# Optimization experiments

Hardware: AMD Instinct MI355X
Metric: run time of the kernel (lower is better)

Reference implementation:

```python
import jax, jax.numpy as jnp
import numpy as np

HEAD_SIZE = 64
N_EMBD = 1024
BLOCK_SIZE = 2048


def setup_inputs() -> dict:
    key = jax.random.key(0)
    ks = jax.random.split(key, 7)
    B, T = 4, 2048
    s = 1.0 / np.sqrt(N_EMBD)
    return {
        "x": jax.random.normal(ks[0], (B, T, N_EMBD), dtype=jnp.float32),
        "Wq": jax.random.normal(ks[1], (N_EMBD, HEAD_SIZE), dtype=jnp.float32) * s,
        "bq": jnp.zeros((HEAD_SIZE,), dtype=jnp.float32),
        "Wk": jax.random.normal(ks[2], (N_EMBD, HEAD_SIZE), dtype=jnp.float32) * s,
        "bk": jnp.zeros((HEAD_SIZE,), dtype=jnp.float32),
        "Wv": jax.random.normal(ks[3], (N_EMBD, HEAD_SIZE), dtype=jnp.float32) * s,
        "bv": jnp.zeros((HEAD_SIZE,), dtype=jnp.float32),
    }


def reference(x, Wq, bq, Wk, bk, Wv, bv):
    # x: [B, T, n_embd]
    B, T, _ = x.shape
    q = x @ Wq + bq  # [B, T, H]
    k = x @ Wk + bk
    v = x @ Wv + bv
    # Faithful to source: divides by head_size**(-0.5) == multiplies by sqrt(head_size)
    scale = jnp.float32(HEAD_SIZE) ** 0.5
    scores = jnp.einsum("bqh,bkh->bqk", q, k) * scale  # [B, T, T]
    causal = jnp.tril(jnp.ones((T, T), dtype=bool))
    scores = jnp.where(causal, scores, -jnp.inf)
    attn = jax.nn.softmax(scores, axis=-1)  # dropout p=0.0 (eval)
    out = jnp.einsum("bqk,bkh->bqh", attn, v)  # [B, T, H]
    return out
```

## Files before the change

kernel.cpp:

```cpp
#include <hip/hip_runtime.h>
#include <math.h>

#define NE 1024
#define HS 64
#define TT 2048
#define QSC 11.541560327111707f

typedef __bf16    v8bf __attribute__((ext_vector_type(8)));
typedef _Float16  v8h  __attribute__((ext_vector_type(8)));
typedef float     v4f  __attribute__((ext_vector_type(4)));

#define MFMA_BF(a, b, c)  __builtin_amdgcn_mfma_f32_16x16x32_bf16((a), (b), (c), 0, 0, 0)
#define MFMA_F16(a, b, c) __builtin_amdgcn_mfma_f32_16x16x32_f16((a), (b), (c), 0, 0, 0)

__device__ __forceinline__ void gl_lds16(const void* g, void* l) {
    __builtin_amdgcn_global_load_lds(
        (const __attribute__((address_space(1))) unsigned int*)g,
        (__attribute__((address_space(3))) unsigned int*)l, 16, 0, 0);
}

__global__ __launch_bounds__(256) void prep_w(
    const float* __restrict__ Wq, const float* __restrict__ Wk,
    const float* __restrict__ Wv, char* __restrict__ imgW)
{
    __shared__ float t[64][65];
    const int bx = blockIdx.x, by = blockIdx.y;
    const float* W = (by == 0) ? Wq : ((by == 1) ? Wk : Wv);
    const int tid = threadIdx.x;
    const int cc = tid & 63, r4 = tid >> 6;
    #pragma unroll
    for (int p = 0; p < 16; ++p) {
        const int k = p * 4 + r4;
        t[k][cc] = W[(size_t)(bx * 64 + k) * HS + cc];
    }
    __syncthreads();
    #pragma unroll
    for (int e = 0; e < 4; ++e) {
        const int chunk = tid + e * 256;
        const int s2   = chunk >> 9;
        const int rem  = chunk & 511;
        const int ctl  = rem >> 7;
        const int rem2 = rem & 127;
        const int pl   = rem2 >> 6;
        const int rem3 = rem2 & 63;
        const int c    = rem3 >> 2;
        const int p16  = rem3 & 3;
        const int kb   = s2 * 32 + ((p16 ^ (c & 3)) << 3);
        const int ncol = ctl * 16 + c;
        v8bf o;
        #pragma unroll
        for (int j = 0; j < 8; ++j) {
            const float v = t[kb + j][ncol];
            const __bf16 h = (__bf16)v;
            o[j] = pl ? (__bf16)(v - (float)h) : h;
        }
        *(v8bf*)(imgW + (size_t)(bx * 2 + s2) * 24576
                 + (by * 4 + ctl) * 2048 + pl * 1024 + c * 64 + p16 * 16) = o;
    }
}

__global__ __launch_bounds__(512, 2) void proj(
    const float* __restrict__ x, const char* __restrict__ imgW,
    const float* __restrict__ bq, const float* __restrict__ bk,
    const float* __restrict__ bv,
    __bf16* __restrict__ qh, __bf16* __restrict__ ql,
    __bf16* __restrict__ kh, __bf16* __restrict__ kl,
    _Float16* __restrict__ vt)
{
    __shared__ __align__(16) char sbuf[2][28672];

    const int tid = threadIdx.x, lane = tid & 63, w = tid >> 6;
    const int rg = w & 1, cg = w >> 1;
    const int quad = lane >> 4, l16 = lane & 15;
    const int m0 = blockIdx.x * 32;

    const int xrow = tid >> 3;
    const int xc32 = ((tid & 7) >> 1) ^ (xrow & 3);
    const float* gx = x + (size_t)(m0 + xrow) * NE + xc32 * 8 + (tid & 1) * 4;
    const char*  gw = imgW + (size_t)tid * 16;

    v4f acc[3];
    #pragma unroll
    for (int i = 0; i < 3; ++i) acc[i] = (v4f){0.f, 0.f, 0.f, 0.f};

    #define STAGE(ks, b)  do {                                        \
        char* xb_ = sbuf[(b)];                                        \
        if (tid < 256) gl_lds16(gx + (ks) * 32, xb_ + tid * 16);      \
        const char* gws_ = gw + (size_t)(ks) * 24576;                 \
        gl_lds16(gws_,         xb_ + 4096  + tid * 16);               \
        gl_lds16(gws_ + 8192,  xb_ + 12288 + tid * 16);               \
        gl_lds16(gws_ + 16384, xb_ + 20480 + tid * 16);               \
    } while (0)

    STAGE(0, 0);
    __syncthreads();

    for (int ks = 0; ks < 32; ++ks) {
        const int b = ks & 1;
        if (ks < 31) STAGE(ks + 1, b ^ 1);

        const char* xb = sbuf[b];
        const char* wb = xb + 4096;
        const int rl = rg * 16 + l16;
        const int pA = quad ^ (rl & 3);
        const float4 a0 = *(const float4*)(xb + rl * 128 + pA * 32);
        const float4 a1 = *(const float4*)(xb + rl * 128 + pA * 32 + 16);
        const float av[8] = {a0.x, a0.y, a0.z, a0.w, a1.x, a1.y, a1.z, a1.w};
        v8bf ah, al;
        #pragma unroll
        for (int i = 0; i < 8; ++i) {
            const __bf16 h = (__bf16)av[i];
            ah[i] = h;
            al[i] = (__bf16)(av[i] - (float)h);
        }
        const int wo = l16 * 64 + ((quad ^ (l16 & 3)) << 4);
        #pragma unroll
        for (int j = 0; j < 3; ++j) {
            const char* base = wb + (cg * 3 + j) * 2048 + wo;
            const v8bf bh = *(const v8bf*)(base);
            const v8bf bl = *(const v8bf*)(base + 1024);
            acc[j] = MFMA_BF(ah, bh, acc[j]);
            acc[j] = MFMA_BF(ah, bl, acc[j]);
            acc[j] = MFMA_BF(al, bh, acc[j]);
        }
        __syncthreads();
    }
    #undef STAGE

    #pragma unroll
    for (int j = 0; j < 3; ++j) {
        const int n = cg * 48 + j * 16 + l16;
        const float bias = (n < 64) ? bq[n] : ((n < 128) ? bk[n - 64] : bv[n - 128]);
        #pragma unroll
        for (int reg = 0; reg < 4; ++reg) {
            const int row = m0 + rg * 16 + quad * 4 + reg;
            const float v = acc[j][reg] + bias;
            if (n < 64) {
                const float s = v * QSC;
                const __bf16 hh = (__bf16)s;
                qh[(size_t)row * HS + n] = hh;
                ql[(size_t)row * HS + n] = (__bf16)(s - (float)hh);
            } else if (n < 128) {
                const __bf16 hh = (__bf16)v;
                kh[(size_t)row * HS + n - 64] = hh;
                kl[(size_t)row * HS + n - 64] = (__bf16)(v - (float)hh);
            } else {
                const int b = row >> 11, tt = row & 2047, hc = n - 128;
                vt[((size_t)(b * HS + hc)) * TT + tt] = (_Float16)v;
            }
        }
    }
}

__global__ __launch_bounds__(256) void attn(
    const __bf16* __restrict__ qh, const __bf16* __restrict__ ql,
    const __bf16* __restrict__ kh, const __bf16* __restrict__ kl,
    const _Float16* __restrict__ vt, float* __restrict__ out)
{
    __shared__ __align__(16) char smem_raw[4 * 16 * 68 * 4];
    _Float16* ps = (_Float16*)smem_raw;
    float*    os = (float*)smem_raw;
    __shared__ float sm[4][16], sl[4][16];

    const int tid = threadIdx.x, lane = tid & 63, w = tid >> 6;
    const int quad = lane >> 4, l16 = lane & 15;
    const int b = blockIdx.x & 3, qi = blockIdx.x >> 2;
    const int q0 = (127 - qi) * 16;

    const size_t qrow = ((size_t)b * TT + q0 + l16) * HS;
    const v8bf Qh0 = *(const v8bf*)(qh + qrow + quad * 8);
    const v8bf Qh1 = *(const v8bf*)(qh + qrow + 32 + quad * 8);
    const v8bf Ql0 = *(const v8bf*)(ql + qrow + quad * 8);
    const v8bf Ql1 = *(const v8bf*)(ql + qrow + 32 + quad * 8);

    const v8h vones = {(_Float16)1.f, (_Float16)1.f, (_Float16)1.f, (_Float16)1.f,
                       (_Float16)1.f, (_Float16)1.f, (_Float16)1.f, (_Float16)1.f};

    float mrow[4] = {-3e38f, -3e38f, -3e38f, -3e38f};
    v4f o[4], o4;
    #pragma unroll
    for (int i = 0; i < 4; ++i) o[i] = (v4f){0.f, 0.f, 0.f, 0.f};
    o4 = (v4f){0.f, 0.f, 0.f, 0.f};

    const int irow = q0 + quad * 4;
    const int ntk = (q0 + 16 + 63) >> 6;
    _Float16* pw = ps + w * (16 * 72);

    for (int t = w; t < ntk; t += 4) {
        const int j0 = t * 64;
        v8bf Kh[8], Kl[8];
        v8h  Vf[8];
        #pragma unroll
        for (int nt = 0; nt < 4; ++nt) {
            const size_t krow = ((size_t)b * TT + j0 + nt * 16 + l16) * HS;
            Kh[nt * 2]     = *(const v8bf*)(kh + krow + quad * 8);
            Kh[nt * 2 + 1] = *(const v8bf*)(kh + krow + 32 + quad * 8);
            Kl[nt * 2]     = *(const v8bf*)(kl + krow + quad * 8);
            Kl[nt * 2 + 1] = *(const v8bf*)(kl + krow + 32 + quad * 8);
        }
        #pragma unroll
        for (int nt = 0; nt < 4; ++nt) {
            const size_t vrow = ((size_t)(b * HS + nt * 16 + l16)) * TT + j0;
            Vf[nt * 2]     = *(const v8h*)(vt + vrow + quad * 8);
            Vf[nt * 2 + 1] = *(const v8h*)(vt + vrow + 32 + quad * 8);
        }

        v4f s[4];
        #pragma unroll
        for (int i = 0; i < 4; ++i) s[i] = (v4f){0.f, 0.f, 0.f, 0.f};
        #pragma unroll
        for (int nt = 0; nt < 4; ++nt) {
            s[nt] = MFMA_BF(Qh0, Kh[nt * 2],     s[nt]);
            s[nt] = MFMA_BF(Qh1, Kh[nt * 2 + 1], s[nt]);
            s[nt] = MFMA_BF(Qh0, Kl[nt * 2],     s[nt]);
            s[nt] = MFMA_BF(Qh1, Kl[nt * 2 + 1], s[nt]);
            s[nt] = MFMA_BF(Ql0, Kh[nt * 2],     s[nt]);
            s[nt] = MFMA_BF(Ql1, Kh[nt * 2 + 1], s[nt]);
        }

        float mx[4] = {-3e38f, -3e38f, -3e38f, -3e38f};
        #pragma unroll
        for (int nt = 0; nt < 4; ++nt)
            #pragma unroll
            for (int reg = 0; reg < 4; ++reg) {
                if (j0 + nt * 16 + l16 > irow + reg) s[nt][reg] = -3e38f;
                mx[reg] = fmaxf(mx[reg], s[nt][reg]);
            }
        #pragma unroll
        for (int off = 8; off; off >>= 1)
            #pragma unroll
            for (int reg = 0; reg < 4; ++reg)
                mx[reg] = fmaxf(mx[reg], __shfl_xor(mx[reg], off));

        float al[4];
        #pragma unroll
        for (int reg = 0; reg < 4; ++reg) {
            const float mn = fmaxf(mrow[reg], mx[reg]);
            al[reg] = exp2f(mrow[reg] - mn);
            mrow[reg] = mn;
        }
        #pragma unroll
        for (int nt = 0; nt < 4; ++nt)
            #pragma unroll
            for (int reg = 0; reg < 4; ++reg) {
                const float p = (j0 + nt * 16 + l16 > irow + reg)
                                    ? 0.f : exp2f(s[nt][reg] - mrow[reg]);
                pw[(quad * 4 + reg) * 72 + nt * 16 + l16] = (_Float16)p;
            }
        #pragma unroll
        for (int nt = 0; nt < 4; ++nt)
            #pragma unroll
            for (int reg = 0; reg < 4; ++reg)
                o[nt][reg] *= al[reg];
        #pragma unroll
        for (int reg = 0; reg < 4; ++reg)
            o4[reg] *= al[reg];

        v8h Pa0 = *(const v8h*)(pw + l16 * 72 + quad * 8);
        v8h Pa1 = *(const v8h*)(pw + l16 * 72 + 32 + quad * 8);
        #pragma unroll
        for (int nt = 0; nt < 4; ++nt) {
            o[nt] = MFMA_F16(Pa0, Vf[nt * 2],     o[nt]);
            o[nt] = MFMA_F16(Pa1, Vf[nt * 2 + 1], o[nt]);
        }
        o4 = MFMA_F16(Pa0, vones, o4);
        o4 = MFMA_F16(Pa1, vones, o4);
    }

    if (l16 == 0) {
        #pragma unroll
        for (int reg = 0; reg < 4; ++reg) {
            sm[w][quad * 4 + reg] = mrow[reg];
            sl[w][quad * 4 + reg] = o4[reg];
        }
    }
    __syncthreads();
    float sc[4];
    #pragma unroll
    for (int reg = 0; reg < 4; ++reg) {
        const int r = quad * 4 + reg;
        float M = sm[0][r];
        #pragma unroll
        for (int i = 1; i < 4; ++i) M = fmaxf(M, sm[i][r]);
        sc[reg] = exp2f(mrow[reg] - M);
    }
    float* ow = os + w * (16 * 68);
    #pragma unroll
    for (int nt = 0; nt < 4; ++nt)
        #pragma unroll
        for (int reg = 0; reg < 4; ++reg)
            ow[(quad * 4 + reg) * 68 + nt * 16 + l16] = o[nt][reg] * sc[reg];
    __syncthreads();

    #pragma unroll
    for (int kk = 0; kk < 4; ++kk) {
        const int m = w * 4 + kk;
        float M = sm[0][m];
        #pragma unroll
        for (int i = 1; i < 4; ++i) M = fmaxf(M, sm[i][m]);
        float L = 0.f, val = 0.f;
        #pragma unroll
        for (int i = 0; i < 4; ++i) {
            L   += sl[i][m] * exp2f(sm[i][m] - M);
            val += os[i * (16 * 68) + m * 68 + lane];
        }
        out[((size_t)b * TT + q0 + m) * HS + lane] = val / L;
    }
}

extern "C" void kernel_launch(void* const* d_in, const int* in_sizes, int n_in,
                              void* d_out, int out_size, void* d_ws, size_t ws_size,
                              hipStream_t stream)
{
    const float* x  = (const float*)d_in[0];
    const float* Wq = (const float*)d_in[1];
    const float* bq = (const float*)d_in[2];
    const float* Wk = (const float*)d_in[3];
    const float* bk = (const float*)d_in[4];
    const float* Wv = (const float*)d_in[5];
    const float* bv = (const float*)d_in[6];
    float* out = (float*)d_out;

    const int rows = in_sizes[0] / NE;
    char* p = (char*)d_ws;
    char* imgW = p;                           p += (size_t)32 * 24576;
    __bf16* qhb = (__bf16*)p;                 p += (size_t)rows * HS * 2;
    __bf16* qlb = (__bf16*)p;                 p += (size_t)rows * HS * 2;
    __bf16* khb = (__bf16*)p;                 p += (size_t)rows * HS * 2;
    __bf16* klb = (__bf16*)p;                 p += (size_t)rows * HS * 2;
    _Float16* vtb = (_Float16*)p;             p += (size_t)rows * HS * 2;

    prep_w<<<dim3(16, 3), 256, 0, stream>>>(Wq, Wk, Wv, imgW);
    proj<<<rows / 32, 512, 0, stream>>>(x, imgW, bq, bk, bv,
                                        qhb, qlb, khb, klb, vtb);
    attn<<<rows / 16, 256, 0, stream>>>(qhb, qlb, khb, klb, vtb, out);
}
```

Measured before the change: 147.8 us.

## Prefetch next K tile in attention and halve projection block size

The attention loop now double-buffers K tiles in registers, loading the next tile's K while the current tile's QK MFMAs and softmax run, so global load latency is hidden. It also adds a min-2-blocks launch bound to attn. The projection kernel is reshaped from 512-thread, 32-row blocks to 256-thread, 16-row blocks, doubling the grid and shrinking LDS per block. The extra K buffers raise register pressure, which could cut occupancy or cause spills, and smaller proj blocks reuse each staged weight tile across fewer rows.

After: 154.0 us. 4.2% more time.

```diff
diff --git a/kernel.cpp b/kernel.cpp
--- a/kernel.cpp
+++ b/kernel.cpp
@@ -59,7 +59,7 @@
     }
 }
 
-__global__ __launch_bounds__(512, 2) void proj(
+__global__ __launch_bounds__(256, 2) void proj(
     const float* __restrict__ x, const char* __restrict__ imgW,
     const float* __restrict__ bq, const float* __restrict__ bk,
     const float* __restrict__ bv,
@@ -67,12 +67,11 @@
     __bf16* __restrict__ kh, __bf16* __restrict__ kl,
     _Float16* __restrict__ vt)
 {
-    __shared__ __align__(16) char sbuf[2][28672];
-
-    const int tid = threadIdx.x, lane = tid & 63, w = tid >> 6;
-    const int rg = w & 1, cg = w >> 1;
+    __shared__ __align__(16) char sbuf[2][26624];
+
+    const int tid = threadIdx.x, lane = tid & 63, cg = tid >> 6;
     const int quad = lane >> 4, l16 = lane & 15;
-    const int m0 = blockIdx.x * 32;
+    const int m0 = blockIdx.x * 16;
 
     const int xrow = tid >> 3;
     const int xc32 = ((tid & 7) >> 1) ^ (xrow & 3);
@@ -83,13 +82,13 @@
     #pragma unroll
     for (int i = 0; i < 3; ++i) acc[i] = (v4f){0.f, 0.f, 0.f, 0.f};
 
-    #define STAGE(ks, b)  do {                                        \
-        char* xb_ = sbuf[(b)];                                        \
-        if (tid < 256) gl_lds16(gx + (ks) * 32, xb_ + tid * 16);      \
-        const char* gws_ = gw + (size_t)(ks) * 24576;                 \
-        gl_lds16(gws_,         xb_ + 4096  + tid * 16);               \
-        gl_lds16(gws_ + 8192,  xb_ + 12288 + tid * 16);               \
-        gl_lds16(gws_ + 16384, xb_ + 20480 + tid * 16);               \
+    #define STAGE(ks, b)  do {                                           \
+        char* xb_ = sbuf[(b)];                                           \
+        if (tid < 128) gl_lds16(gx + (ks) * 32, xb_ + tid * 16);         \
+        const char* gws_ = gw + (size_t)(ks) * 24576;                    \
+        _Pragma("unroll")                                                \
+        for (int j_ = 0; j_ < 6; ++j_)                                   \
+            gl_lds16(gws_ + j_ * 4096, xb_ + 2048 + tid * 16 + j_ * 4096); \
     } while (0)
 
     STAGE(0, 0);
@@ -100,8 +99,8 @@
         if (ks < 31) STAGE(ks + 1, b ^ 1);
 
         const char* xb = sbuf[b];
-        const char* wb = xb + 4096;
-        const int rl = rg * 16 + l16;
+        const char* wb = xb + 2048;
+        const int rl = l16;
         const int pA = quad ^ (rl & 3);
         const float4 a0 = *(const float4*)(xb + rl * 128 + pA * 32);
         const float4 a1 = *(const float4*)(xb + rl * 128 + pA * 32 + 16);
@@ -133,7 +132,7 @@
         const float bias = (n < 64) ? bq[n] : ((n < 128) ? bk[n - 64] : bv[n - 128]);
         #pragma unroll
         for (int reg = 0; reg < 4; ++reg) {
-            const int row = m0 + rg * 16 + quad * 4 + reg;
+            const int row = m0 + quad * 4 + reg;
             const float v = acc[j][reg] + bias;
             if (n < 64) {
                 const float s = v * QSC;
@@ -145,14 +144,14 @@
                 kh[(size_t)row * HS + n - 64] = hh;
                 kl[(size_t)row * HS + n - 64] = (__bf16)(v - (float)hh);
             } else {
-                const int b = row >> 11, tt = row & 2047, hc = n - 128;
-                vt[((size_t)(b * HS + hc)) * TT + tt] = (_Float16)v;
+                const int b2 = row >> 11, tt = row & 2047, hc = n - 128;
+                vt[((size_t)(b2 * HS + hc)) * TT + tt] = (_Float16)v;
             }
         }
     }
 }
 
-__global__ __launch_bounds__(256) void attn(
+__global__ __launch_bounds__(256, 2) void attn(
     const __bf16* __restrict__ qh, const __bf16* __restrict__ ql,
     const __bf16* __restrict__ kh, const __bf16* __restrict__ kl,
     const _Float16* __restrict__ vt, float* __restrict__ out)
@@ -186,38 +185,38 @@
     const int ntk = (q0 + 16 + 63) >> 6;
     _Float16* pw = ps + w * (16 * 72);
 
-    for (int t = w; t < ntk; t += 4) {
-        const int j0 = t * 64;
-        v8bf Kh[8], Kl[8];
-        v8h  Vf[8];
+    auto loadK = [&](v8bf (&Kh_)[8], v8bf (&Kl_)[8], int j0) {
         #pragma unroll
         for (int nt = 0; nt < 4; ++nt) {
             const size_t krow = ((size_t)b * TT + j0 + nt * 16 + l16) * HS;
-            Kh[nt * 2]     = *(const v8bf*)(kh + krow + quad * 8);
-            Kh[nt * 2 + 1] = *(const v8bf*)(kh + krow + 32 + quad * 8);
-            Kl[nt * 2]     = *(const v8bf*)(kl + krow + quad * 8);
-            Kl[nt * 2 + 1] = *(const v8bf*)(kl + krow + 32 + quad * 8);
-        }
+            Kh_[nt * 2]     = *(const v8bf*)(kh + krow + quad * 8);
+            Kh_[nt * 2 + 1] = *(const v8bf*)(kh + krow + 32 + quad * 8);
+            Kl_[nt * 2]     = *(const v8bf*)(kl + krow + quad * 8);
+            Kl_[nt * 2 + 1] = *(const v8bf*)(kl + krow + 32 + quad * 8);
+        }
+    };
+    auto loadV = [&](v8h (&Vf_)[8], int j0) {
         #pragma unroll
         for (int nt = 0; nt < 4; ++nt) {
             const size_t vrow = ((size_t)(b * HS + nt * 16 + l16)) * TT + j0;
-            Vf[nt * 2]     = *(const v8h*)(vt + vrow + quad * 8);
-            Vf[nt * 2 + 1] = *(const v8h*)(vt + vrow + 32 + quad * 8);
-        }
-
-        v4f s[4];
+            Vf_[nt * 2]     = *(const v8h*)(vt + vrow + quad * 8);
+            Vf_[nt * 2 + 1] = *(const v8h*)(vt + vrow + 32 + quad * 8);
+        }
+    };
+    auto qkmm = [&](v8bf (&Kh_)[8], v8bf (&Kl_)[8], v4f (&s)[4]) {
         #pragma unroll
         for (int i = 0; i < 4; ++i) s[i] = (v4f){0.f, 0.f, 0.f, 0.f};
         #pragma unroll
         for (int nt = 0; nt < 4; ++nt) {
-            s[nt] = MFMA_BF(Qh0, Kh[nt * 2],     s[nt]);
-            s[nt] = MFMA_BF(Qh1, Kh[nt * 2 + 1], s[nt]);
-            s[nt] = MFMA_BF(Qh0, Kl[nt * 2],     s[nt]);
-            s[nt] = MFMA_BF(Qh1, Kl[nt * 2 + 1], s[nt]);
-            s[nt] = MFMA_BF(Ql0, Kh[nt * 2],     s[nt]);
-            s[nt] = MFMA_BF(Ql1, Kh[nt * 2 + 1], s[nt]);
-        }
-
+            s[nt] = MFMA_BF(Qh0, Kh_[nt * 2],     s[nt]);
+            s[nt] = MFMA_BF(Qh1, Kh_[nt * 2 + 1], s[nt]);
+            s[nt] = MFMA_BF(Qh0, Kl_[nt * 2],     s[nt]);
+            s[nt] = MFMA_BF(Qh1, Kl_[nt * 2 + 1], s[nt]);
+            s[nt] = MFMA_BF(Ql0, Kh_[nt * 2],     s[nt]);
+            s[nt] = MFMA_BF(Ql1, Kh_[nt * 2 + 1], s[nt]);
+        }
+    };
+    auto smaxpv = [&](v4f (&s)[4], v8h (&Vf_)[8], int j0) {
         float mx[4] = {-3e38f, -3e38f, -3e38f, -3e38f};
         #pragma unroll
         for (int nt = 0; nt < 4; ++nt)
@@ -231,7 +230,6 @@
             #pragma unroll
             for (int reg = 0; reg < 4; ++reg)
                 mx[reg] = fmaxf(mx[reg], __shfl_xor(mx[reg], off));
-
         float al[4];
         #pragma unroll
         for (int reg = 0; reg < 4; ++reg) {
@@ -255,16 +253,38 @@
         #pragma unroll
         for (int reg = 0; reg < 4; ++reg)
             o4[reg] *= al[reg];
-
         v8h Pa0 = *(const v8h*)(pw + l16 * 72 + quad * 8);
         v8h Pa1 = *(const v8h*)(pw + l16 * 72 + 32 + quad * 8);
         #pragma unroll
         for (int nt = 0; nt < 4; ++nt) {
-            o[nt] = MFMA_F16(Pa0, Vf[nt * 2],     o[nt]);
-            o[nt] = MFMA_F16(Pa1, Vf[nt * 2 + 1], o[nt]);
+            o[nt] = MFMA_F16(Pa0, Vf_[nt * 2],     o[nt]);
+            o[nt] = MFMA_F16(Pa1, Vf_[nt * 2 + 1], o[nt]);
         }
         o4 = MFMA_F16(Pa0, vones, o4);
         o4 = MFMA_F16(Pa1, vones, o4);
+    };
+
+    v8bf KhA[8], KlA[8], KhB[8], KlB[8];
+    v8h  Vf[8];
+    v4f  s[4];
+
+    int t = w;
+    if (t < ntk) {
+        loadK(KhA, KlA, t * 64);
+        for (;;) {
+            loadV(Vf, t * 64);
+            qkmm(KhA, KlA, s);
+            if (t + 4 < ntk) loadK(KhB, KlB, (t + 4) * 64);
+            smaxpv(s, Vf, t * 64);
+            t += 4;
+            if (t >= ntk) break;
+            loadV(Vf, t * 64);
+            qkmm(KhB, KlB, s);
+            if (t + 4 < ntk) loadK(KhA, KlA, (t + 4) * 64);
+            smaxpv(s, Vf, t * 64);
+            t += 4;
+            if (t >= ntk) break;
+        }
     }
 
     if (l16 == 0) {
@@ -331,7 +351,7 @@
     _Float16* vtb = (_Float16*)p;             p += (size_t)rows * HS * 2;
 
     prep_w<<<dim3(16, 3), 256, 0, stream>>>(Wq, Wk, Wv, imgW);
-    proj<<<rows / 32, 512, 0, stream>>>(x, imgW, bq, bk, bv,
+    proj<<<rows / 16, 256, 0, stream>>>(x, imgW, bq, bk, bv,
                                         qhb, qlb, khb, klb, vtb);
     attn<<<rows / 16, 256, 0, stream>>>(qhb, qlb, khb, klb, vtb, out);
 }
```

## Pair causal query tiles per attention block and shrink projection blocks

Applied to the files above, without the earlier changes.

The attention kernel now pairs a long causal query tile (from the end of the sequence) with a short one (from the start) in each 512-thread block. Eight waves split the combined KV chunks, which balances work across blocks and halves the grid. The final reduction over 8 waves now uses a larger LDS buffer (68 KB). The projection kernel goes from 32-row, 512-thread blocks to 16-row, 256-thread blocks, giving more blocks but with each weight tile re-read by twice as many blocks.

Result: faster. 138.7 us (-6.2%).

```diff
diff --git a/kernel.cpp b/kernel.cpp
--- a/kernel.cpp
+++ b/kernel.cpp
@@ -59,7 +59,7 @@
     }
 }
 
-__global__ __launch_bounds__(512, 2) void proj(
+__global__ __launch_bounds__(256, 2) void proj(
     const float* __restrict__ x, const char* __restrict__ imgW,
     const float* __restrict__ bq, const float* __restrict__ bk,
     const float* __restrict__ bv,
@@ -67,12 +67,11 @@
     __bf16* __restrict__ kh, __bf16* __restrict__ kl,
     _Float16* __restrict__ vt)
 {
-    __shared__ __align__(16) char sbuf[2][28672];
-
-    const int tid = threadIdx.x, lane = tid & 63, w = tid >> 6;
-    const int rg = w & 1, cg = w >> 1;
+    __shared__ __align__(16) char sbuf[2][26624];
+
+    const int tid = threadIdx.x, lane = tid & 63, cg = tid >> 6;
     const int quad = lane >> 4, l16 = lane & 15;
-    const int m0 = blockIdx.x * 32;
+    const int m0 = blockIdx.x * 16;
 
     const int xrow = tid >> 3;
     const int xc32 = ((tid & 7) >> 1) ^ (xrow & 3);
@@ -83,13 +82,13 @@
     #pragma unroll
     for (int i = 0; i < 3; ++i) acc[i] = (v4f){0.f, 0.f, 0.f, 0.f};
 
-    #define STAGE(ks, b)  do {                                        \
-        char* xb_ = sbuf[(b)];                                        \
-        if (tid < 256) gl_lds16(gx + (ks) * 32, xb_ + tid * 16);      \
-        const char* gws_ = gw + (size_t)(ks) * 24576;                 \
-        gl_lds16(gws_,         xb_ + 4096  + tid * 16);               \
-        gl_lds16(gws_ + 8192,  xb_ + 12288 + tid * 16);               \
-        gl_lds16(gws_ + 16384, xb_ + 20480 + tid * 16);               \
+    #define STAGE(ks, b)  do {                                           \
+        char* xb_ = sbuf[(b)];                                           \
+        if (tid < 128) gl_lds16(gx + (ks) * 32, xb_ + tid * 16);         \
+        const char* gws_ = gw + (size_t)(ks) * 24576;                    \
+        _Pragma("unroll")                                                \
+        for (int j_ = 0; j_ < 6; ++j_)                                   \
+            gl_lds16(gws_ + j_ * 4096, xb_ + 2048 + tid * 16 + j_ * 4096); \
     } while (0)
 
     STAGE(0, 0);
@@ -100,8 +99,8 @@
         if (ks < 31) STAGE(ks + 1, b ^ 1);
 
         const char* xb = sbuf[b];
-        const char* wb = xb + 4096;
-        const int rl = rg * 16 + l16;
+        const char* wb = xb + 2048;
+        const int rl = l16;
         const int pA = quad ^ (rl & 3);
         const float4 a0 = *(const float4*)(xb + rl * 128 + pA * 32);
         const float4 a1 = *(const float4*)(xb + rl * 128 + pA * 32 + 16);
@@ -133,7 +132,7 @@
         const float bias = (n < 64) ? bq[n] : ((n < 128) ? bk[n - 64] : bv[n - 128]);
         #pragma unroll
         for (int reg = 0; reg < 4; ++reg) {
-            const int row = m0 + rg * 16 + quad * 4 + reg;
+            const int row = m0 + quad * 4 + reg;
             const float v = acc[j][reg] + bias;
             if (n < 64) {
                 const float s = v * QSC;
@@ -145,49 +144,59 @@
                 kh[(size_t)row * HS + n - 64] = hh;
                 kl[(size_t)row * HS + n - 64] = (__bf16)(v - (float)hh);
             } else {
-                const int b = row >> 11, tt = row & 2047, hc = n - 128;
-                vt[((size_t)(b * HS + hc)) * TT + tt] = (_Float16)v;
+                const int b2 = row >> 11, tt = row & 2047, hc = n - 128;
+                vt[((size_t)(b2 * HS + hc)) * TT + tt] = (_Float16)v;
             }
         }
     }
 }
 
-__global__ __launch_bounds__(256) void attn(
+__global__ __launch_bounds__(512, 2) void attn(
     const __bf16* __restrict__ qh, const __bf16* __restrict__ ql,
     const __bf16* __restrict__ kh, const __bf16* __restrict__ kl,
     const _Float16* __restrict__ vt, float* __restrict__ out)
 {
-    __shared__ __align__(16) char smem_raw[4 * 16 * 68 * 4];
+    __shared__ __align__(16) char smem_raw[69632];
     _Float16* ps = (_Float16*)smem_raw;
     float*    os = (float*)smem_raw;
-    __shared__ float sm[4][16], sl[4][16];
+    __shared__ float sm[8][2][16], sl[8][2][16];
 
     const int tid = threadIdx.x, lane = tid & 63, w = tid >> 6;
     const int quad = lane >> 4, l16 = lane & 15;
-    const int b = blockIdx.x & 3, qi = blockIdx.x >> 2;
-    const int q0 = (127 - qi) * 16;
-
-    const size_t qrow = ((size_t)b * TT + q0 + l16) * HS;
-    const v8bf Qh0 = *(const v8bf*)(qh + qrow + quad * 8);
-    const v8bf Qh1 = *(const v8bf*)(qh + qrow + 32 + quad * 8);
-    const v8bf Ql0 = *(const v8bf*)(ql + qrow + quad * 8);
-    const v8bf Ql1 = *(const v8bf*)(ql + qrow + 32 + quad * 8);
+    const int b = blockIdx.x & 3, pair = blockIdx.x >> 2;
+    const int q0t[2] = {(127 - pair) * 16, pair * 16};
+    const int ntk0 = (q0t[0] + 16 + 63) >> 6;
+    const int ntk1 = (q0t[1] + 16 + 63) >> 6;
+    const int total = ntk0 + ntk1;
+
+    v8bf Qh0[2], Qh1[2], Ql0[2], Ql1[2];
+    #pragma unroll
+    for (int t = 0; t < 2; ++t) {
+        const size_t qrow = ((size_t)b * TT + q0t[t] + l16) * HS;
+        Qh0[t] = *(const v8bf*)(qh + qrow + quad * 8);
+        Qh1[t] = *(const v8bf*)(qh + qrow + 32 + quad * 8);
+        Ql0[t] = *(const v8bf*)(ql + qrow + quad * 8);
+        Ql1[t] = *(const v8bf*)(ql + qrow + 32 + quad * 8);
+    }
 
     const v8h vones = {(_Float16)1.f, (_Float16)1.f, (_Float16)1.f, (_Float16)1.f,
                        (_Float16)1.f, (_Float16)1.f, (_Float16)1.f, (_Float16)1.f};
 
-    float mrow[4] = {-3e38f, -3e38f, -3e38f, -3e38f};
-    v4f o[4], o4;
-    #pragma unroll
-    for (int i = 0; i < 4; ++i) o[i] = (v4f){0.f, 0.f, 0.f, 0.f};
-    o4 = (v4f){0.f, 0.f, 0.f, 0.f};
-
-    const int irow = q0 + quad * 4;
-    const int ntk = (q0 + 16 + 63) >> 6;
+    float mr0[4] = {-3e38f, -3e38f, -3e38f, -3e38f};
+    float mr1[4] = {-3e38f, -3e38f, -3e38f, -3e38f};
+    v4f o0[4], o1[4], l40, l41;
+    #pragma unroll
+    for (int i = 0; i < 4; ++i) {
+        o0[i] = (v4f){0.f, 0.f, 0.f, 0.f};
+        o1[i] = (v4f){0.f, 0.f, 0.f, 0.f};
+    }
+    l40 = (v4f){0.f, 0.f, 0.f, 0.f};
+    l41 = (v4f){0.f, 0.f, 0.f, 0.f};
+
     _Float16* pw = ps + w * (16 * 72);
 
-    for (int t = w; t < ntk; t += 4) {
-        const int j0 = t * 64;
+    auto doChunk = [&](int j0, int q0c, int t,
+                       float (&mrow)[4], v4f (&o)[4], v4f &o4) {
         v8bf Kh[8], Kl[8];
         v8h  Vf[8];
         #pragma unroll
@@ -204,20 +213,19 @@
             Vf[nt * 2]     = *(const v8h*)(vt + vrow + quad * 8);
             Vf[nt * 2 + 1] = *(const v8h*)(vt + vrow + 32 + quad * 8);
         }
-
         v4f s[4];
         #pragma unroll
         for (int i = 0; i < 4; ++i) s[i] = (v4f){0.f, 0.f, 0.f, 0.f};
         #pragma unroll
         for (int nt = 0; nt < 4; ++nt) {
-            s[nt] = MFMA_BF(Qh0, Kh[nt * 2],     s[nt]);
-            s[nt] = MFMA_BF(Qh1, Kh[nt * 2 + 1], s[nt]);
-            s[nt] = MFMA_BF(Qh0, Kl[nt * 2],     s[nt]);
-            s[nt] = MFMA_BF(Qh1, Kl[nt * 2 + 1], s[nt]);
-            s[nt] = MFMA_BF(Ql0, Kh[nt * 2],     s[nt]);
-            s[nt] = MFMA_BF(Ql1, Kh[nt * 2 + 1], s[nt]);
-        }
-
+            s[nt] = MFMA_BF(Qh0[t], Kh[nt * 2],     s[nt]);
+            s[nt] = MFMA_BF(Qh1[t], Kh[nt * 2 + 1], s[nt]);
+            s[nt] = MFMA_BF(Qh0[t], Kl[nt * 2],     s[nt]);
+            s[nt] = MFMA_BF(Qh1[t], Kl[nt * 2 + 1], s[nt]);
+            s[nt] = MFMA_BF(Ql0[t], Kh[nt * 2],     s[nt]);
+            s[nt] = MFMA_BF(Ql1[t], Kh[nt * 2 + 1], s[nt]);
+        }
+        const int irow = q0c + quad * 4;
         float mx[4] = {-3e38f, -3e38f, -3e38f, -3e38f};
         #pragma unroll
         for (int nt = 0; nt < 4; ++nt)
@@ -231,7 +239,6 @@
             #pragma unroll
             for (int reg = 0; reg < 4; ++reg)
                 mx[reg] = fmaxf(mx[reg], __shfl_xor(mx[reg], off));
-
         float al[4];
         #pragma unroll
         for (int reg = 0; reg < 4; ++reg) {
@@ -255,9 +262,8 @@
         #pragma unroll
         for (int reg = 0; reg < 4; ++reg)
             o4[reg] *= al[reg];
-
-        v8h Pa0 = *(const v8h*)(pw + l16 * 72 + quad * 8);
-        v8h Pa1 = *(const v8h*)(pw + l16 * 72 + 32 + quad * 8);
+        const v8h Pa0 = *(const v8h*)(pw + l16 * 72 + quad * 8);
+        const v8h Pa1 = *(const v8h*)(pw + l16 * 72 + 32 + quad * 8);
         #pragma unroll
         for (int nt = 0; nt < 4; ++nt) {
             o[nt] = MFMA_F16(Pa0, Vf[nt * 2],     o[nt]);
@@ -265,46 +271,61 @@
         }
         o4 = MFMA_F16(Pa0, vones, o4);
         o4 = MFMA_F16(Pa1, vones, o4);
+    };
+
+    for (int c = w; c < total; c += 8) {
+        if (c < ntk0) doChunk(c * 64,          q0t[0], 0, mr0, o0, l40);
+        else          doChunk((c - ntk0) * 64, q0t[1], 1, mr1, o1, l41);
     }
 
     if (l16 == 0) {
         #pragma unroll
         for (int reg = 0; reg < 4; ++reg) {
-            sm[w][quad * 4 + reg] = mrow[reg];
-            sl[w][quad * 4 + reg] = o4[reg];
+            sm[w][0][quad * 4 + reg] = mr0[reg];
+            sl[w][0][quad * 4 + reg] = l40[reg];
+            sm[w][1][quad * 4 + reg] = mr1[reg];
+            sl[w][1][quad * 4 + reg] = l41[reg];
         }
     }
     __syncthreads();
-    float sc[4];
-    #pragma unroll
-    for (int reg = 0; reg < 4; ++reg) {
-        const int r = quad * 4 + reg;
-        float M = sm[0][r];
-        #pragma unroll
-        for (int i = 1; i < 4; ++i) M = fmaxf(M, sm[i][r]);
-        sc[reg] = exp2f(mrow[reg] - M);
-    }
-    float* ow = os + w * (16 * 68);
-    #pragma unroll
-    for (int nt = 0; nt < 4; ++nt)
-        #pragma unroll
-        for (int reg = 0; reg < 4; ++reg)
-            ow[(quad * 4 + reg) * 68 + nt * 16 + l16] = o[nt][reg] * sc[reg];
+
+    #pragma unroll
+    for (int t = 0; t < 2; ++t) {
+        float sc[4];
+        #pragma unroll
+        for (int reg = 0; reg < 4; ++reg) {
+            const int r = quad * 4 + reg;
+            float M = sm[0][t][r];
+            #pragma unroll
+            for (int i = 1; i < 8; ++i) M = fmaxf(M, sm[i][t][r]);
+            const float mw = t ? mr1[reg] : mr0[reg];
+            sc[reg] = exp2f(mw - M);
+        }
+        float* ow = os + (size_t)(w * 2 + t) * (16 * 68);
+        #pragma unroll
+        for (int nt = 0; nt < 4; ++nt)
+            #pragma unroll
+            for (int reg = 0; reg < 4; ++reg) {
+                const v4f& oo = t ? o1[nt] : o0[nt];
+                ow[(quad * 4 + reg) * 68 + nt * 16 + l16] = oo[reg] * sc[reg];
+            }
+    }
     __syncthreads();
 
     #pragma unroll
     for (int kk = 0; kk < 4; ++kk) {
-        const int m = w * 4 + kk;
-        float M = sm[0][m];
-        #pragma unroll
-        for (int i = 1; i < 4; ++i) M = fmaxf(M, sm[i][m]);
+        const int g = w * 4 + kk;
+        const int t = g >> 4, m = g & 15;
+        float M = sm[0][t][m];
+        #pragma unroll
+        for (int i = 1; i < 8; ++i) M = fmaxf(M, sm[i][t][m]);
         float L = 0.f, val = 0.f;
         #pragma unroll
-        for (int i = 0; i < 4; ++i) {
-            L   += sl[i][m] * exp2f(sm[i][m] - M);
-            val += os[i * (16 * 68) + m * 68 + lane];
-        }
-        out[((size_t)b * TT + q0 + m) * HS + lane] = val / L;
+        for (int i = 0; i < 8; ++i) {
+            L   += sl[i][t][m] * exp2f(sm[i][t][m] - M);
+            val += os[(size_t)(i * 2 + t) * (16 * 68) + m * 68 + lane];
+        }
+        out[((size_t)b * TT + q0t[t] + m) * HS + lane] = val / L;
     }
 }
 
@@ -331,7 +352,7 @@
     _Float16* vtb = (_Float16*)p;             p += (size_t)rows * HS * 2;
 
     prep_w<<<dim3(16, 3), 256, 0, stream>>>(Wq, Wk, Wv, imgW);
-    proj<<<rows / 32, 512, 0, stream>>>(x, imgW, bq, bk, bv,
+    proj<<<rows / 16, 256, 0, stream>>>(x, imgW, bq, bk, bv,
                                         qhb, qlb, khb, klb, vtb);
-    attn<<<rows / 16, 256, 0, stream>>>(qhb, qlb, khb, klb, vtb, out);
-}
+    attn<<<rows / 32, 512, 0, stream>>>(qhb, qlb, khb, klb, vtb, out);
+}
```
